# Performance work log

Measured on AMD Instinct MI355X. Metric: run time of the kernel, lower is better.

## Reference

```python
import jax, jax.numpy as jnp
import numpy as np

N_FILTERS = 40
FILTER_SIZE = 401   # int(16000*25/1000), forced odd
POOL_STRIDE = 160   # int(16000*10/1000)
EPS = 1e-6
S_SMOOTH = 0.04     # fixed PCEN smoothing coefficient s
DELTA = 2.0         # fixed PCEN bias delta
R_MIN, R_MAX = 0.2, 1.0
HIDDEN = 32


def setup_inputs() -> dict:
    key = jax.random.key(0)
    ks = jax.random.split(key, 6)
    B, L = 8, 160000
    x = jax.random.normal(ks[0], (B, L), dtype=jnp.float32)
    # mel-initialized Gabor params (as in mel_filter_params)
    sr, fmin, fmax = 16000.0, 60.0, 7800.0
    min_mel = 1127.0 * np.log1p(fmin / 700.0)
    max_mel = 1127.0 * np.log1p(fmax / 700.0)
    peaks_mel = np.linspace(min_mel, max_mel, N_FILTERS + 2)
    peaks_hz = 700.0 * np.expm1(peaks_mel / 1127.0)
    center_freqs = jnp.asarray(peaks_hz[1:-1] * 2.0 * np.pi / sr, dtype=jnp.float32)
    z = np.sqrt(2.0 * np.log(2.0)) / np.pi
    bandwidths = jnp.asarray(z * sr / (peaks_hz[2:] - peaks_hz[:-2]), dtype=jnp.float32)
    pooling_widths = jnp.full((N_FILTERS,), 0.4, dtype=jnp.float32)
    # GRU (input_size=1, hidden=32) + head Linear(32,32)->ReLU->Linear(32,2)
    def gl(k, shape):
        return jax.random.normal(k, shape, dtype=jnp.float32) * 0.1
    w_ih = gl(ks[1], (3 * HIDDEN, 1))
    w_hh = gl(ks[2], (3 * HIDDEN, HIDDEN))
    b_ih = jnp.zeros((3 * HIDDEN,), jnp.float32)
    b_hh = jnp.zeros((3 * HIDDEN,), jnp.float32)
    hw1 = gl(ks[3], (32, HIDDEN)); hb1 = jnp.zeros((32,), jnp.float32)
    hw2 = gl(ks[4], (2, 32)); hb2 = jnp.zeros((2,), jnp.float32)
    return dict(x=x, center_freqs=center_freqs, bandwidths=bandwidths,
                pooling_widths=pooling_widths, w_ih=w_ih, w_hh=w_hh,
                b_ih=b_ih, b_hh=b_hh, hw1=hw1, hb1=hb1, hw2=hw2, hb2=hb2)


def _gabor_filterbank(x, center_freqs, bandwidths, pooling_widths):
    z = np.sqrt(2.0 * np.log(2.0)) / np.pi
    cf = jnp.clip(center_freqs, 0.0, np.pi)
    bw = jnp.clip(bandwidths, 4.0 * z, FILTER_SIZE * z)
    t = jnp.arange(-(FILTER_SIZE // 2), (FILTER_SIZE + 1) // 2, dtype=jnp.float32)
    denom = 1.0 / (jnp.sqrt(2.0 * np.pi) * bw)                        # [F]
    gauss = jnp.exp(-(t[None, :] ** 2) / (2.0 * bw[:, None] ** 2))    # [F,K]
    phase = cf[:, None] * t[None, :]                                  # [F,K]
    fr = denom[:, None] * gauss * jnp.cos(phase)
    fi = denom[:, None] * gauss * jnp.sin(phase)
    filt = jnp.concatenate([fr, fi], axis=0)[:, None, :]              # [2F,1,K]
    pad = FILTER_SIZE // 2
    y = jax.lax.conv_general_dilated(x[:, None, :], filt, (1,), [(pad, pad)])
    y = y ** 2
    y = y[:, :N_FILTERS] + y[:, N_FILTERS:]                           # squared modulus [B,F,L]
    pw = jnp.clip(pooling_widths, 2.0 / FILTER_SIZE, 0.5)
    tt = jnp.arange(FILTER_SIZE, dtype=jnp.float32) / (FILTER_SIZE - 1) - 0.5
    win = jnp.exp(-0.5 * (tt[None, :] / pw[:, None]) ** 2)[:, None, :]  # [F,1,K]
    y = jax.lax.conv_general_dilated(y, win, (POOL_STRIDE,), [(pad, pad)],
                                     feature_group_count=N_FILTERS)
    return y  # [B,F,T]


def _gru_cell(h, xin, w_ih, w_hh, b_ih, b_hh):
    gi = xin @ w_ih.T + b_ih   # [N,3H]
    gh = h @ w_hh.T + b_hh
    i_r, i_z, i_n = jnp.split(gi, 3, axis=-1)
    h_r, h_z, h_n = jnp.split(gh, 3, axis=-1)
    r = jax.nn.sigmoid(i_r + h_r)
    zz = jax.nn.sigmoid(i_z + h_z)
    n = jnp.tanh(i_n + r * h_n)
    return (1.0 - zz) * n + zz * h


def _adaptive_pcen(frames, w_ih, w_hh, b_ih, b_hh, hw1, hb1, hw2, hb2):
    B, F, T = frames.shape
    Xt = jnp.transpose(frames, (2, 0, 1))  # [T,B,F]

    def controller(x_prev, x_t):  # each [B,F] -> per-bin (alpha, r)
        xp = x_prev.reshape(-1, 1)
        xc = x_t.reshape(-1, 1)
        h = jnp.zeros((B * F, HIDDEN), frames.dtype)
        h = _gru_cell(h, xp, w_ih, w_hh, b_ih, b_hh)
        h = _gru_cell(h, xc, w_ih, w_hh, b_ih, b_hh)
        hid = jax.nn.relu(h @ hw1.T + hb1)
        logits = hid @ hw2.T + hb2  # [B*F,2]
        alpha = jax.nn.sigmoid(logits[:, 0]).reshape(B, F)
        r = (R_MIN + (R_MAX - R_MIN) * jax.nn.sigmoid(logits[:, 1])).reshape(B, F)
        return alpha, r

    def step(carry, X_t):
        M_prev, X_prev = carry
        alpha, r = controller(X_prev, X_t)
        M_t = (1.0 - S_SMOOTH) * M_prev + S_SMOOTH * X_t
        out = (X_t / (M_t + EPS) ** alpha + DELTA) ** r - DELTA ** r
        return (M_t, X_t), out

    init = (jnp.zeros((B, F), frames.dtype), Xt[0])
    _, outs = jax.lax.scan(step, init, Xt)
    return jnp.transpose(outs, (1, 2, 0))  # [B,F,T]


def reference(x, center_freqs, bandwidths, pooling_widths,
              w_ih, w_hh, b_ih, b_hh, hw1, hb1, hw2, hb2):
    frames = _gabor_filterbank(x, center_freqs, bandwidths, pooling_widths)
    return _adaptive_pcen(frames, w_ih, w_hh, b_ih, b_hh, hw1, hb1, hw2, hb2)
```

## Files before the change

### kernel.cpp

```cpp
#include <hip/hip_runtime.h>
#include <math.h>

#define NF 40
#define FS 401
#define AST 424
#define PSTRIDE 160
#define BB 8
#define LL 160000
#define PADL 256
#define LST 160512
#define TOUT 1000
#define NTILE 256
#define NCHUNKC 625
#define ROWCH 89
#define ROWST (ROWCH*8)
#define TCP 16
#define NCHUNKP 63

typedef __attribute__((ext_vector_type(8))) _Float16 half8v;
typedef __attribute__((ext_vector_type(4))) _Float16 half4v;
typedef __attribute__((ext_vector_type(4))) float float4v;
typedef _Float16 f16;

__device__ __forceinline__ float sigm(float x) { return 1.0f / (1.0f + __expf(-x)); }
__device__ __forceinline__ float tanh_fast(float x) { return 1.0f - 2.0f / (__expf(2.0f * x) + 1.0f); }

__global__ __launch_bounds__(256) void prep_filters(
    const float* __restrict__ cf_, const float* __restrict__ bw_, f16* __restrict__ Ag)
{
    const float PI_F = 3.14159265358979323846f;
    int row = blockIdx.x;
    int f = row >> 1, comp = row & 1;
    float Z = sqrtf(2.0f * logf(2.0f)) / PI_F;
    float cf = fminf(fmaxf(cf_[f], 0.0f), PI_F);
    float bw = fminf(fmaxf(bw_[f], 4.0f * Z), 401.0f * Z);
    float denom = 1.0f / (sqrtf(2.0f * PI_F) * bw);
    float inv2 = 1.0f / (2.0f * bw * bw);
    for (int k = threadIdx.x; k < AST; k += 256) {
        float v = 0.0f;
        if (k < FS) {
            float t = (float)(k - 200);
            float g = denom * expf(-(t * t) * inv2);
            float sv, cv;
            sincosf(cf * t, &sv, &cv);
            v = comp ? g * sv : g * cv;
        }
        Ag[row * AST + k] = (f16)v;
    }
}

__global__ __launch_bounds__(256) void convert_x(
    const float* __restrict__ x, f16* __restrict__ xb)
{
    int i = blockIdx.x * 256 + threadIdx.x;
    if (i >= BB * LST) return;
    int b = i / LST, o = i % LST;
    float v = 0.0f;
    if (o >= PADL && o < PADL + LL) v = x[b * LL + (o - PADL)];
    xb[i] = (f16)v;
}

__global__ __launch_bounds__(256) void conv_mfma(
    const f16* __restrict__ xb,
    const f16* __restrict__ Ag,
    f16* __restrict__ eb)
{
    __shared__ f16 rows_[8 * ROWST];
    int chunk = blockIdx.x;
    int bi = blockIdx.y;
    int p0 = chunk * NTILE;
    int pbase = PADL + p0 - 200;
    const f16* xs = xb + (size_t)bi * LST;
    int tid = threadIdx.x;

    for (int sc = tid; sc < 8 * 84; sc += 256) {
        int r = sc / 84, m = sc - r * 84;
        int s0 = pbase + 8 * m + (r & ~1);
        const uint* gp = (const uint*)(xs + s0);
        uint v0 = gp[0], v1 = gp[1], v2 = gp[2], v3 = gp[3], v4 = gp[4];
        if (r & 1) {
            v0 = __builtin_amdgcn_alignbyte(v1, v0, 2);
            v1 = __builtin_amdgcn_alignbyte(v2, v1, 2);
            v2 = __builtin_amdgcn_alignbyte(v3, v2, 2);
            v3 = __builtin_amdgcn_alignbyte(v4, v3, 2);
        }
        *(uint4*)(&rows_[r * ROWST + 8 * m]) = make_uint4(v0, v1, v2, v3);
    }
    __syncthreads();

    int wv = tid >> 6, lane = tid & 63, q = lane >> 4, l15 = lane & 15;

    float4v acc[5][4];
#pragma unroll
    for (int t = 0; t < 5; ++t)
#pragma unroll
        for (int s = 0; s < 4; ++s)
            acc[t][s] = (float4v){0.f, 0.f, 0.f, 0.f};

    const f16* aP[5];
    const f16* bP[4];
#pragma unroll
    for (int t = 0; t < 5; ++t) aP[t] = Ag + (16 * t + l15) * AST + 8 * q;
#pragma unroll
    for (int s = 0; s < 4; ++s) {
        int pos = 64 * wv + 16 * s + l15;
        bP[s] = rows_ + (pos & 7) * ROWST + 8 * ((pos >> 3) + q);
    }

    for (int k = 0; k < 416; k += 32) {
        half8v af[5], bf[4];
#pragma unroll
        for (int t = 0; t < 5; ++t) af[t] = *(const half8v*)(aP[t] + k);
#pragma unroll
        for (int s = 0; s < 4; ++s) bf[s] = *(const half8v*)(bP[s] + k);
#pragma unroll
        for (int t = 0; t < 5; ++t)
#pragma unroll
            for (int s = 0; s < 4; ++s)
                acc[t][s] = __builtin_amdgcn_mfma_f32_16x16x32_f16(af[t], bf[s], acc[t][s], 0, 0, 0);
    }

    f16* ebb = eb + (size_t)bi * NF * LL;
#pragma unroll
    for (int t = 0; t < 5; ++t) {
        int f0 = 8 * t + 2 * q;
#pragma unroll
        for (int s = 0; s < 4; ++s) {
            float4v a = acc[t][s];
            int p = p0 + 64 * wv + 16 * s + l15;
            float e0 = a.x * a.x + a.y * a.y;
            float e1 = a.z * a.z + a.w * a.w;
            ebb[f0 * LL + p] = (f16)e0;
            ebb[(f0 + 1) * LL + p] = (f16)e1;
        }
    }
}

__global__ __launch_bounds__(256) void pool_kernel(
    const f16* __restrict__ eb, const float* __restrict__ pw_, float* __restrict__ Xout)
{
    __shared__ float ys[2816];
    __shared__ float win[416];
    int chunk = blockIdx.x;
    int f = blockIdx.y;
    int bi = blockIdx.z;
    int tau0 = chunk * TCP;
    int start = tau0 * PSTRIDE - 200;
    int tid = threadIdx.x;

    float pw = fminf(fmaxf(pw_[f], 2.0f / 401.0f), 0.5f);
    float invpw = 1.0f / pw;
    for (int k = tid; k < 416; k += 256) {
        float w = 0.0f;
        if (k < FS) {
            float tt = (float)k * (1.0f / 400.0f) - 0.5f;
            float u = tt * invpw;
            w = expf(-0.5f * u * u);
        }
        win[k] = w;
    }
    const f16* erow = eb + ((size_t)bi * NF + f) * LL;
    if (start >= 0 && start + 2816 <= LL) {
        for (int j = tid; j < 352; j += 256) {
            half8v v = *(const half8v*)(erow + start + 8 * j);
#pragma unroll
            for (int i = 0; i < 8; ++i) ys[8 * j + i] = (float)v[i];
        }
    } else {
        for (int j = tid; j < 2816; j += 256) {
            int p = start + j;
            ys[j] = (p >= 0 && p < LL) ? (float)erow[p] : 0.0f;
        }
    }
    __syncthreads();

    int ft = tid >> 4, l16 = tid & 15;
    float acc = 0.0f;
    int yo = ft * PSTRIDE;
    for (int kw = l16; kw < FS; kw += 16)
        acc += ys[yo + kw] * win[kw];
#pragma unroll
    for (int off = 8; off > 0; off >>= 1)
        acc += __shfl_down(acc, off, 16);
    int tau = tau0 + ft;
    if (l16 == 0 && tau < TOUT)
        Xout[((size_t)bi * NF + f) * TOUT + tau] = acc;
}

__global__ __launch_bounds__(256) void pcen_scan_kernel(
    const float* __restrict__ X, float* __restrict__ M)
{
    int wid = (blockIdx.x * 256 + threadIdx.x) >> 6;
    int lane = threadIdx.x & 63;
    if (wid >= BB * NF) return;
    const float a1 = 0.96f;
    const float a2 = a1 * a1;
    const float a4 = a2 * a2;
    const float a8 = a4 * a4;
    const float a16 = a8 * a8;
    const float a32 = a16 * a16;
    const float ss = 0.04f;
    float al1 = powf(a1, (float)(lane + 1));
    float carry = 0.0f;
    const float* row = X + wid * TOUT;
    float* mrow = M + wid * TOUT;

    for (int c = 0; c < TOUT; c += 64) {
        int t = c + lane;
        float v = (t < TOUT) ? row[t] : 0.0f;
        float y = ss * v;
        float u;
        u = __shfl_up(y, 1, 64);  if (lane >= 1)  y = fmaf(a1, u, y);
        u = __shfl_up(y, 2, 64);  if (lane >= 2)  y = fmaf(a2, u, y);
        u = __shfl_up(y, 4, 64);  if (lane >= 4)  y = fmaf(a4, u, y);
        u = __shfl_up(y, 8, 64);  if (lane >= 8)  y = fmaf(a8, u, y);
        u = __shfl_up(y, 16, 64); if (lane >= 16) y = fmaf(a16, u, y);
        u = __shfl_up(y, 32, 64); if (lane >= 32) y = fmaf(a32, u, y);
        y = fmaf(al1, carry, y);
        carry = __shfl(y, 63, 64);
        if (t < TOUT) mrow[t] = y;
    }
}

__global__ __launch_bounds__(256) void pcen_ctrl_mfma(
    const float* __restrict__ X, const float* __restrict__ M,
    const float* __restrict__ w_ih, const float* __restrict__ w_hh,
    const float* __restrict__ b_ih, const float* __restrict__ b_hh,
    const float* __restrict__ hw1, const float* __restrict__ hb1,
    const float* __restrict__ hw2, const float* __restrict__ hb2,
    float* __restrict__ out)
{
    __shared__ f16 s_whhA[96 * 40];
    __shared__ f16 s_w1A[32 * 40];
    __shared__ __align__(16) float4 s_A1[32];
    __shared__ __align__(16) float4 s_A2[32];
    __shared__ float s_hb1[32];
    __shared__ float s_hw2[64];
    __shared__ float s_hb2[2];
    __shared__ f16 sh1[4][16 * 40];
    __shared__ f16 sh2[4][16 * 40];
    __shared__ float sxc[4][16], sxp[4][16], smv[4][16];

    int tid = threadIdx.x;
    for (int i = tid; i < 96 * 32; i += 256) {
        int m = i >> 5, k = i & 31;
        s_whhA[m * 40 + k] = (f16)w_hh[i];
    }
    for (int i = tid; i < 32 * 32; i += 256) {
        int m = i >> 5, k = i & 31;
        s_w1A[m * 40 + k] = (f16)hw1[i];
    }
    if (tid < 32) {
        int j = tid;
        s_A1[j] = make_float4(w_ih[j], b_ih[j] + b_hh[j],
                              w_ih[32 + j], b_ih[32 + j] + b_hh[32 + j]);
        s_A2[j] = make_float4(w_ih[64 + j], b_ih[64 + j], b_hh[64 + j], 0.0f);
        s_hb1[j] = hb1[j];
    }
    if (tid < 64) s_hw2[tid] = hw2[tid];
    if (tid < 2)  s_hb2[tid] = hb2[tid];
    __syncthreads();

    int wv = tid >> 6, lane = tid & 63;
    int c = lane & 15, q = lane >> 4;
    int instBase = blockIdx.x * 64 + wv * 16;

    if (lane < 16) {
        int idx = instBase + lane;
        int t = idx % TOUT;
        float xcv = X[idx];
        float xpv = (t == 0) ? xcv : X[idx - 1];
        sxc[wv][lane] = xcv;
        sxp[wv][lane] = xpv;
        smv[wv][lane] = M[idx];
    }
    float xp = sxp[wv][c];
    float xc = sxc[wv][c];
    float mv = smv[wv][c];

    float h1v[8];
#pragma unroll
    for (int jj = 0; jj < 8; ++jj) {
        int j = (jj < 4) ? (4 * q + jj) : (16 + 4 * q + (jj - 4));
        float4 a1 = s_A1[j];
        float4 a2 = s_A2[j];
        float r = sigm(fmaf(xp, a1.x, a1.y));
        float z = sigm(fmaf(xp, a1.z, a1.w));
        float n = tanh_fast(fmaf(xp, a2.x, a2.y) + r * a2.z);
        h1v[jj] = (1.0f - z) * n;
    }

    {
        half4v lo = {(f16)h1v[0], (f16)h1v[1], (f16)h1v[2], (f16)h1v[3]};
        half4v hi = {(f16)h1v[4], (f16)h1v[5], (f16)h1v[6], (f16)h1v[7]};
        *(half4v*)(&sh1[wv][c * 40 + 4 * q]) = lo;
        *(half4v*)(&sh1[wv][c * 40 + 16 + 4 * q]) = hi;
    }

    float4v acc[6];
    {
        half8v bf = *(const half8v*)(&sh1[wv][c * 40 + 8 * q]);
#pragma unroll
        for (int t = 0; t < 6; ++t) {
            half8v af = *(const half8v*)(&s_whhA[(16 * t + c) * 40 + 8 * q]);
            acc[t] = __builtin_amdgcn_mfma_f32_16x16x32_f16(af, bf, (float4v){0.f,0.f,0.f,0.f}, 0, 0, 0);
        }
    }

    float h2v[8];
#pragma unroll
    for (int jj = 0; jj < 8; ++jj) {
        int j = (jj < 4) ? (4 * q + jj) : (16 + 4 * q + (jj - 4));
        int reg = jj & 3;
        float accR = (jj < 4) ? acc[0][reg] : acc[1][reg];
        float accZ = (jj < 4) ? acc[2][reg] : acc[3][reg];
        float accN = (jj < 4) ? acc[4][reg] : acc[5][reg];
        float4 a1 = s_A1[j];
        float4 a2 = s_A2[j];
        float r = sigm(fmaf(xc, a1.x, a1.y) + accR);
        float z = sigm(fmaf(xc, a1.z, a1.w) + accZ);
        float gn = accN + a2.z;
        float n = tanh_fast(fmaf(xc, a2.x, a2.y) + r * gn);
        h2v[jj] = fmaf(z, h1v[jj] - n, n);
    }

    {
        half4v lo = {(f16)h2v[0], (f16)h2v[1], (f16)h2v[2], (f16)h2v[3]};
        half4v hi = {(f16)h2v[4], (f16)h2v[5], (f16)h2v[6], (f16)h2v[7]};
        *(half4v*)(&sh2[wv][c * 40 + 4 * q]) = lo;
        *(half4v*)(&sh2[wv][c * 40 + 16 + 4 * q]) = hi;
    }

    float4v hacc[2];
    {
        half8v bf = *(const half8v*)(&sh2[wv][c * 40 + 8 * q]);
#pragma unroll
        for (int t = 0; t < 2; ++t) {
            half8v af = *(const half8v*)(&s_w1A[(16 * t + c) * 40 + 8 * q]);
            hacc[t] = __builtin_amdgcn_mfma_f32_16x16x32_f16(af, bf, (float4v){0.f,0.f,0.f,0.f}, 0, 0, 0);
        }
    }

    float p0 = 0.f, p1 = 0.f;
#pragma unroll
    for (int jj = 0; jj < 8; ++jj) {
        int i = (jj < 4) ? (4 * q + jj) : (16 + 4 * q + (jj - 4));
        int reg = jj & 3;
        float hv = (jj < 4) ? hacc[0][reg] : hacc[1][reg];
        hv = fmaxf(hv + s_hb1[i], 0.0f);
        p0 = fmaf(hv, s_hw2[i], p0);
        p1 = fmaf(hv, s_hw2[32 + i], p1);
    }
    p0 += __shfl_xor(p0, 16);
    p0 += __shfl_xor(p0, 32);
    p1 += __shfl_xor(p1, 16);
    p1 += __shfl_xor(p1, 32);

    float alpha = sigm(p0 + s_hb2[0]);
    float rr = fmaf(0.8f, sigm(p1 + s_hb2[1]), 0.2f);
    float md = __expf(alpha * __logf(mv + 1e-6f));
    float bse = xc / md + 2.0f;
    float val = __expf(rr * __logf(bse)) - __expf(rr * 0.69314718056f);
    if (lane < 16)
        out[instBase + lane] = val;
}

extern "C" void kernel_launch(void* const* d_in, const int* in_sizes, int n_in,
                              void* d_out, int out_size, void* d_ws, size_t ws_size,
                              hipStream_t stream) {
    const float* x    = (const float*)d_in[0];
    const float* cf   = (const float*)d_in[1];
    const float* bw   = (const float*)d_in[2];
    const float* pw   = (const float*)d_in[3];
    const float* w_ih = (const float*)d_in[4];
    const float* w_hh = (const float*)d_in[5];
    const float* b_ih = (const float*)d_in[6];
    const float* b_hh = (const float*)d_in[7];
    const float* hw1  = (const float*)d_in[8];
    const float* hb1  = (const float*)d_in[9];
    const float* hw2  = (const float*)d_in[10];
    const float* hb2  = (const float*)d_in[11];
    float* out = (float*)d_out;

    const size_t xb_b  = (size_t)BB * LST * 2;
    const size_t ag_b  = (size_t)80 * AST * 2;
    const size_t xm_b  = (size_t)2 * BB * NF * TOUT * 4;
    size_t fixed = xb_b + ag_b + xm_b;
    size_t e_per_batch = (size_t)NF * LL * 2;
    int nb;
    if (ws_size >= fixed + 8 * e_per_batch)      nb = 8;
    else if (ws_size >= fixed + 2 * e_per_batch) nb = 2;
    else                                         nb = 1;
    int nslice = BB / nb;

    f16* xb   = (f16*)d_ws;
    f16* Ag   = xb + (size_t)BB * LST;
    f16* ebuf = Ag + (size_t)80 * AST;
    float* Xf = (float*)(ebuf + (size_t)nb * NF * LL);
    float* Mf = Xf + (size_t)BB * NF * TOUT;

    prep_filters<<<dim3(80), dim3(256), 0, stream>>>(cf, bw, Ag);
    convert_x<<<dim3((BB * LST + 255) / 256), dim3(256), 0, stream>>>(x, xb);

    for (int sl = 0; sl < nslice; ++sl) {
        conv_mfma<<<dim3(NCHUNKC, nb), dim3(256), 0, stream>>>(
            xb + (size_t)sl * nb * LST, Ag, ebuf);
        pool_kernel<<<dim3(NCHUNKP, NF, nb), dim3(256), 0, stream>>>(
            ebuf, pw, Xf + (size_t)sl * nb * NF * TOUT);
    }

    pcen_scan_kernel<<<dim3((BB * NF * 64) / 256), dim3(256), 0, stream>>>(Xf, Mf);
    pcen_ctrl_mfma<<<dim3((BB * NF * TOUT) / 64), dim3(256), 0, stream>>>(
        Xf, Mf, w_ih, w_hh, b_ih, b_hh, hw1, hb1, hw2, hb2, out);
}
```

Measured before the change: 293.3 us.

## Fuse Gabor conv energy with Gaussian pooling via LDS and atomic accumulation

Merges the conv_mfma and pool_kernel passes into one kernel. Each block computes squared-magnitude energies for a 512-sample tile into LDS and pools them directly with atomicAdd partial sums into the frame output. This removes the large f16 energy buffer written to and read back from global memory, and the per-slice launch loop. The tile per block doubles, which raises register pressure (40 accumulators per lane), and it adds a memset, a window-precompute kernel and float atomics whose summation order is nondeterministic. The pooling loop is scalar and serial per thread, and only 240 of 256 threads do it.

New measurement: 312.2 us. 1.06x slower.

```diff
diff --git a/kernel.cpp b/kernel.cpp
--- a/kernel.cpp
+++ b/kernel.cpp
@@ -8,14 +8,16 @@
 #define BB 8
 #define LL 160000
 #define PADL 256
-#define LST 160512
+#define PADR 512
+#define LST 160768
 #define TOUT 1000
-#define NTILE 256
-#define NCHUNKC 625
-#define ROWCH 89
+#define NTILE 512
+#define NCHUNKC 313
+#define ROWCH 121
 #define ROWST (ROWCH*8)
-#define TCP 16
-#define NCHUNKP 63
+#define EST 518
+#define WST 402
+#define WOFF 41472
 
 typedef __attribute__((ext_vector_type(8))) _Float16 half8v;
 typedef __attribute__((ext_vector_type(4))) _Float16 half4v;
@@ -49,6 +51,23 @@
     }
 }
 
+__global__ __launch_bounds__(256) void prep_win(
+    const float* __restrict__ pw_, f16* __restrict__ winG)
+{
+    int f = blockIdx.x;
+    float pw = fminf(fmaxf(pw_[f], 2.0f / 401.0f), 0.5f);
+    float invpw = 1.0f / pw;
+    for (int j = threadIdx.x; j < WST; j += 256) {
+        float w = 0.0f;
+        if (j < FS) {
+            float tt = (float)j * (1.0f / 400.0f) - 0.5f;
+            float u = tt * invpw;
+            w = expf(-0.5f * u * u);
+        }
+        winG[f * WST + j] = (f16)w;
+    }
+}
+
 __global__ __launch_bounds__(256) void convert_x(
     const float* __restrict__ x, f16* __restrict__ xb)
 {
@@ -60,12 +79,17 @@
     xb[i] = (f16)v;
 }
 
-__global__ __launch_bounds__(256) void conv_mfma(
+__global__ __launch_bounds__(256, 2) void conv_pool(
     const f16* __restrict__ xb,
     const f16* __restrict__ Ag,
-    f16* __restrict__ eb)
-{
-    __shared__ f16 rows_[8 * ROWST];
+    const f16* __restrict__ winG,
+    float* __restrict__ Xout)
+{
+    __shared__ __align__(16) unsigned char smem[WOFF + 20 * WST * 2];
+    f16* slab = (f16*)smem;
+    f16* eL   = (f16*)smem;
+    f16* wL   = (f16*)(smem + WOFF);
+
     int chunk = blockIdx.x;
     int bi = blockIdx.y;
     int p0 = chunk * NTILE;
@@ -73,8 +97,8 @@
     const f16* xs = xb + (size_t)bi * LST;
     int tid = threadIdx.x;
 
-    for (int sc = tid; sc < 8 * 84; sc += 256) {
-        int r = sc / 84, m = sc - r * 84;
+    for (int sc = tid; sc < 8 * 117; sc += 256) {
+        int r = sc / 117, m = sc - r * 117;
         int s0 = pbase + 8 * m + (r & ~1);
         const uint* gp = (const uint*)(xs + s0);
         uint v0 = gp[0], v1 = gp[1], v2 = gp[2], v3 = gp[3], v4 = gp[4];
@@ -84,107 +108,89 @@
             v2 = __builtin_amdgcn_alignbyte(v3, v2, 2);
             v3 = __builtin_amdgcn_alignbyte(v4, v3, 2);
         }
-        *(uint4*)(&rows_[r * ROWST + 8 * m]) = make_uint4(v0, v1, v2, v3);
+        *(uint4*)(&slab[r * ROWST + 8 * m]) = make_uint4(v0, v1, v2, v3);
     }
     __syncthreads();
 
     int wv = tid >> 6, lane = tid & 63, q = lane >> 4, l15 = lane & 15;
 
-    float4v acc[5][4];
+    float4v acc[5][8];
 #pragma unroll
     for (int t = 0; t < 5; ++t)
 #pragma unroll
-        for (int s = 0; s < 4; ++s)
+        for (int s = 0; s < 8; ++s)
             acc[t][s] = (float4v){0.f, 0.f, 0.f, 0.f};
 
     const f16* aP[5];
-    const f16* bP[4];
+    const f16* bP[8];
 #pragma unroll
     for (int t = 0; t < 5; ++t) aP[t] = Ag + (16 * t + l15) * AST + 8 * q;
 #pragma unroll
-    for (int s = 0; s < 4; ++s) {
-        int pos = 64 * wv + 16 * s + l15;
-        bP[s] = rows_ + (pos & 7) * ROWST + 8 * ((pos >> 3) + q);
+    for (int s = 0; s < 8; ++s) {
+        int pos = 128 * wv + 16 * s + l15;
+        bP[s] = slab + (pos & 7) * ROWST + 8 * ((pos >> 3) + q);
     }
 
     for (int k = 0; k < 416; k += 32) {
-        half8v af[5], bf[4];
+        half8v af[5], bf[8];
 #pragma unroll
         for (int t = 0; t < 5; ++t) af[t] = *(const half8v*)(aP[t] + k);
 #pragma unroll
-        for (int s = 0; s < 4; ++s) bf[s] = *(const half8v*)(bP[s] + k);
+        for (int s = 0; s < 8; ++s) bf[s] = *(const half8v*)(bP[s] + k);
 #pragma unroll
         for (int t = 0; t < 5; ++t)
 #pragma unroll
-            for (int s = 0; s < 4; ++s)
+            for (int s = 0; s < 8; ++s)
                 acc[t][s] = __builtin_amdgcn_mfma_f32_16x16x32_f16(af[t], bf[s], acc[t][s], 0, 0, 0);
     }
 
-    f16* ebb = eb + (size_t)bi * NF * LL;
+    __syncthreads();
+
 #pragma unroll
     for (int t = 0; t < 5; ++t) {
         int f0 = 8 * t + 2 * q;
 #pragma unroll
-        for (int s = 0; s < 4; ++s) {
+        for (int s = 0; s < 8; ++s) {
             float4v a = acc[t][s];
-            int p = p0 + 64 * wv + 16 * s + l15;
-            float e0 = a.x * a.x + a.y * a.y;
-            float e1 = a.z * a.z + a.w * a.w;
-            ebb[f0 * LL + p] = (f16)e0;
-            ebb[(f0 + 1) * LL + p] = (f16)e1;
-        }
-    }
-}
-
-__global__ __launch_bounds__(256) void pool_kernel(
-    const f16* __restrict__ eb, const float* __restrict__ pw_, float* __restrict__ Xout)
-{
-    __shared__ float ys[2816];
-    __shared__ float win[416];
-    int chunk = blockIdx.x;
-    int f = blockIdx.y;
-    int bi = blockIdx.z;
-    int tau0 = chunk * TCP;
-    int start = tau0 * PSTRIDE - 200;
-    int tid = threadIdx.x;
-
-    float pw = fminf(fmaxf(pw_[f], 2.0f / 401.0f), 0.5f);
-    float invpw = 1.0f / pw;
-    for (int k = tid; k < 416; k += 256) {
-        float w = 0.0f;
-        if (k < FS) {
-            float tt = (float)k * (1.0f / 400.0f) - 0.5f;
-            float u = tt * invpw;
-            w = expf(-0.5f * u * u);
-        }
-        win[k] = w;
-    }
-    const f16* erow = eb + ((size_t)bi * NF + f) * LL;
-    if (start >= 0 && start + 2816 <= LL) {
-        for (int j = tid; j < 352; j += 256) {
-            half8v v = *(const half8v*)(erow + start + 8 * j);
-#pragma unroll
-            for (int i = 0; i < 8; ++i) ys[8 * j + i] = (float)v[i];
-        }
-    } else {
-        for (int j = tid; j < 2816; j += 256) {
-            int p = start + j;
-            ys[j] = (p >= 0 && p < LL) ? (float)erow[p] : 0.0f;
+            int pl = 128 * wv + 16 * s + l15;
+            eL[f0 * EST + pl] = (f16)(a.x * a.x + a.y * a.y);
+            eL[(f0 + 1) * EST + pl] = (f16)(a.z * a.z + a.w * a.w);
         }
     }
     __syncthreads();
 
-    int ft = tid >> 4, l16 = tid & 15;
-    float acc = 0.0f;
-    int yo = ft * PSTRIDE;
-    for (int kw = l16; kw < FS; kw += 16)
-        acc += ys[yo + kw] * win[kw];
-#pragma unroll
-    for (int off = 8; off > 0; off >>= 1)
-        acc += __shfl_down(acc, off, 16);
-    int tau = tau0 + ft;
-    if (l16 == 0 && tau < TOUT)
-        Xout[((size_t)bi * NF + f) * TOUT + tau] = acc;
+    int tau_lo = (p0 > 200) ? (p0 - 200 + 159) / 160 : 0;
+    float* Xb = Xout + (size_t)bi * NF * TOUT;
+
+    for (int ph = 0; ph < 2; ++ph) {
+        const uint4* src = (const uint4*)(winG + ph * 20 * WST);
+        uint4* dst = (uint4*)wL;
+        for (int u = tid; u < (20 * WST * 2) / 16; u += 256) dst[u] = src[u];
+        __syncthreads();
+
+        if (tid < 240) {
+            int fl = tid / 12, r = tid % 12, ti = r >> 1, h = r & 1;
+            int f = ph * 20 + fl;
+            int tau = tau_lo + ti;
+            if (tau < TOUT) {
+                int base = tau * PSTRIDE - 200;
+                int jlo = max(0, p0 - base);
+                int jhi = min(401, p0 + NTILE - base);
+                int jm = (jlo + jhi + 1) >> 1;
+                int ja = h ? jm : jlo;
+                int jb = h ? jhi : jm;
+                if (ja < jb) {
+                    float a = 0.0f;
+                    const f16* er = eL + f * EST + (base - p0);
+                    const f16* wr = wL + fl * WST;
+                    for (int j = ja; j < jb; ++j)
+                        a = fmaf((float)er[j], (float)wr[j], a);
+                    atomicAdd(&Xb[f * TOUT + tau], a);
+                }
+            }
+        }
+        __syncthreads();
+    }
 }
 
 __global__ __launch_bounds__(256) void pcen_scan_kernel(
@@ -382,32 +388,18 @@
     const float* hb2  = (const float*)d_in[11];
     float* out = (float*)d_out;
 
-    const size_t xb_b  = (size_t)BB * LST * 2;
-    const size_t ag_b  = (size_t)80 * AST * 2;
-    const size_t xm_b  = (size_t)2 * BB * NF * TOUT * 4;
-    size_t fixed = xb_b + ag_b + xm_b;
-    size_t e_per_batch = (size_t)NF * LL * 2;
-    int nb;
-    if (ws_size >= fixed + 8 * e_per_batch)      nb = 8;
-    else if (ws_size >= fixed + 2 * e_per_batch) nb = 2;
-    else                                         nb = 1;
-    int nslice = BB / nb;
-
-    f16* xb   = (f16*)d_ws;
-    f16* Ag   = xb + (size_t)BB * LST;
-    f16* ebuf = Ag + (size_t)80 * AST;
-    float* Xf = (float*)(ebuf + (size_t)nb * NF * LL);
-    float* Mf = Xf + (size_t)BB * NF * TOUT;
+    f16* xb    = (f16*)d_ws;
+    f16* Ag    = xb + (size_t)BB * LST;
+    f16* winG  = Ag + (size_t)80 * AST;
+    float* Xf  = (float*)(winG + (size_t)NF * WST);
+    float* Mf  = Xf + (size_t)BB * NF * TOUT;
 
     prep_filters<<<dim3(80), dim3(256), 0, stream>>>(cf, bw, Ag);
+    prep_win<<<dim3(NF), dim3(256), 0, stream>>>(pw, winG);
     convert_x<<<dim3((BB * LST + 255) / 256), dim3(256), 0, stream>>>(x, xb);
-
-    for (int sl = 0; sl < nslice; ++sl) {
-        conv_mfma<<<dim3(NCHUNKC, nb), dim3(256), 0, stream>>>(
-            xb + (size_t)sl * nb * LST, Ag, ebuf);
-        pool_kernel<<<dim3(NCHUNKP, NF, nb), dim3(256), 0, stream>>>(
-            ebuf, pw, Xf + (size_t)sl * nb * NF * TOUT);
-    }
+    hipMemsetAsync(Xf, 0, (size_t)BB * NF * TOUT * sizeof(float), stream);
+
+    conv_pool<<<dim3(NCHUNKC, BB), dim3(256), 0, stream>>>(xb, Ag, winG, Xf);
 
     pcen_scan_kernel<<<dim3((BB * NF * 64) / 256), dim3(256), 0, stream>>>(Xf, Mf);
     pcen_ctrl_mfma<<<dim3((BB * NF * TOUT) / 64), dim3(256), 0, stream>>>(
```

## Double conv MFMA output tile per block and merge prep kernels into one launch

Applied to the files above, without the earlier changes.

The convolution tile grows from 256 to 512 output positions per block. Each wave now computes 8 position subtiles, so every filter A-fragment loaded is reused across twice as many MFMAs, and the shared-memory slab grows to match. The input padding is widened and a bounds check guards the partial last tile. The x-to-f16 conversion and filter preparation are merged into a single launch to remove one kernel launch. The trade-off is more accumulator registers (occupancy is pinned at 2 blocks per CU via launch bounds) and fewer blocks in the grid.

Measured after the change: 310.8 us. 1.06x slower.

```diff
diff --git a/kernel.cpp b/kernel.cpp
--- a/kernel.cpp
+++ b/kernel.cpp
@@ -8,14 +8,16 @@
 #define BB 8
 #define LL 160000
 #define PADL 256
-#define LST 160512
+#define PADR 512
+#define LST 160768
 #define TOUT 1000
-#define NTILE 256
-#define NCHUNKC 625
-#define ROWCH 89
+#define NTILE 512
+#define NCHUNKC 313
+#define ROWCH 121
 #define ROWST (ROWCH*8)
 #define TCP 16
 #define NCHUNKP 63
+#define NCONVB 5024
 
 typedef __attribute__((ext_vector_type(8))) _Float16 half8v;
 typedef __attribute__((ext_vector_type(4))) _Float16 half4v;
@@ -25,11 +27,21 @@
 __device__ __forceinline__ float sigm(float x) { return 1.0f / (1.0f + __expf(-x)); }
 __device__ __forceinline__ float tanh_fast(float x) { return 1.0f - 2.0f / (__expf(2.0f * x) + 1.0f); }
 
-__global__ __launch_bounds__(256) void prep_filters(
-    const float* __restrict__ cf_, const float* __restrict__ bw_, f16* __restrict__ Ag)
+__global__ __launch_bounds__(256) void prep_all(
+    const float* __restrict__ x, const float* __restrict__ cf_,
+    const float* __restrict__ bw_, f16* __restrict__ xb, f16* __restrict__ Ag)
 {
+    int blk = blockIdx.x;
+    if (blk < NCONVB) {
+        int i = blk * 256 + threadIdx.x;
+        int b = i / LST, o = i % LST;
+        float v = 0.0f;
+        if (o >= PADL && o < PADL + LL) v = x[b * LL + (o - PADL)];
+        xb[i] = (f16)v;
+        return;
+    }
     const float PI_F = 3.14159265358979323846f;
-    int row = blockIdx.x;
+    int row = blk - NCONVB;
     int f = row >> 1, comp = row & 1;
     float Z = sqrtf(2.0f * logf(2.0f)) / PI_F;
     float cf = fminf(fmaxf(cf_[f], 0.0f), PI_F);
@@ -49,23 +61,12 @@
     }
 }
 
-__global__ __launch_bounds__(256) void convert_x(
-    const float* __restrict__ x, f16* __restrict__ xb)
-{
-    int i = blockIdx.x * 256 + threadIdx.x;
-    if (i >= BB * LST) return;
-    int b = i / LST, o = i % LST;
-    float v = 0.0f;
-    if (o >= PADL && o < PADL + LL) v = x[b * LL + (o - PADL)];
-    xb[i] = (f16)v;
-}
-
-__global__ __launch_bounds__(256) void conv_mfma(
+__global__ __launch_bounds__(256, 2) void conv_mfma(
     const f16* __restrict__ xb,
     const f16* __restrict__ Ag,
     f16* __restrict__ eb)
 {
-    __shared__ f16 rows_[8 * ROWST];
+    __shared__ f16 slab[8 * ROWST];
     int chunk = blockIdx.x;
     int bi = blockIdx.y;
     int p0 = chunk * NTILE;
@@ -73,8 +74,8 @@
     const f16* xs = xb + (size_t)bi * LST;
     int tid = threadIdx.x;
 
-    for (int sc = tid; sc < 8 * 84; sc += 256) {
-        int r = sc / 84, m = sc - r * 84;
+    for (int sc = tid; sc < 8 * 117; sc += 256) {
+        int r = sc / 117, m = sc - r * 117;
         int s0 = pbase + 8 * m + (r & ~1);
         const uint* gp = (const uint*)(xs + s0);
         uint v0 = gp[0], v1 = gp[1], v2 = gp[2], v3 = gp[3], v4 = gp[4];
@@ -84,39 +85,39 @@
             v2 = __builtin_amdgcn_alignbyte(v3, v2, 2);
             v3 = __builtin_amdgcn_alignbyte(v4, v3, 2);
         }
-        *(uint4*)(&rows_[r * ROWST + 8 * m]) = make_uint4(v0, v1, v2, v3);
+        *(uint4*)(&slab[r * ROWST + 8 * m]) = make_uint4(v0, v1, v2, v3);
     }
     __syncthreads();
 
     int wv = tid >> 6, lane = tid & 63, q = lane >> 4, l15 = lane & 15;
 
-    float4v acc[5][4];
+    float4v acc[5][8];
 #pragma unroll
     for (int t = 0; t < 5; ++t)
 #pragma unroll
-        for (int s = 0; s < 4; ++s)
+        for (int s = 0; s < 8; ++s)
             acc[t][s] = (float4v){0.f, 0.f, 0.f, 0.f};
 
     const f16* aP[5];
-    const f16* bP[4];
+    const f16* bP[8];
 #pragma unroll
     for (int t = 0; t < 5; ++t) aP[t] = Ag + (16 * t + l15) * AST + 8 * q;
 #pragma unroll
-    for (int s = 0; s < 4; ++s) {
-        int pos = 64 * wv + 16 * s + l15;
-        bP[s] = rows_ + (pos & 7) * ROWST + 8 * ((pos >> 3) + q);
+    for (int s = 0; s < 8; ++s) {
+        int pos = 128 * wv + 16 * s + l15;
+        bP[s] = slab + (pos & 7) * ROWST + 8 * ((pos >> 3) + q);
     }
 
     for (int k = 0; k < 416; k += 32) {
-        half8v af[5], bf[4];
+        half8v af[5], bf[8];
 #pragma unroll
         for (int t = 0; t < 5; ++t) af[t] = *(const half8v*)(aP[t] + k);
 #pragma unroll
-        for (int s = 0; s < 4; ++s) bf[s] = *(const half8v*)(bP[s] + k);
+        for (int s = 0; s < 8; ++s) bf[s] = *(const half8v*)(bP[s] + k);
 #pragma unroll
         for (int t = 0; t < 5; ++t)
 #pragma unroll
-            for (int s = 0; s < 4; ++s)
+            for (int s = 0; s < 8; ++s)
                 acc[t][s] = __builtin_amdgcn_mfma_f32_16x16x32_f16(af[t], bf[s], acc[t][s], 0, 0, 0);
     }
 
@@ -125,13 +126,13 @@
     for (int t = 0; t < 5; ++t) {
         int f0 = 8 * t + 2 * q;
 #pragma unroll
-        for (int s = 0; s < 4; ++s) {
+        for (int s = 0; s < 8; ++s) {
             float4v a = acc[t][s];
-            int p = p0 + 64 * wv + 16 * s + l15;
-            float e0 = a.x * a.x + a.y * a.y;
-            float e1 = a.z * a.z + a.w * a.w;
-            ebb[f0 * LL + p] = (f16)e0;
-            ebb[(f0 + 1) * LL + p] = (f16)e1;
+            int p = p0 + 128 * wv + 16 * s + l15;
+            if (p < LL) {
+                ebb[f0 * LL + p] = (f16)(a.x * a.x + a.y * a.y);
+                ebb[(f0 + 1) * LL + p] = (f16)(a.z * a.z + a.w * a.w);
+            }
         }
     }
 }
@@ -382,9 +383,9 @@
     const float* hb2  = (const float*)d_in[11];
     float* out = (float*)d_out;
 
-    const size_t xb_b  = (size_t)BB * LST * 2;
-    const size_t ag_b  = (size_t)80 * AST * 2;
-    const size_t xm_b  = (size_t)2 * BB * NF * TOUT * 4;
+    const size_t xb_b = (size_t)BB * LST * 2;
+    const size_t ag_b = (size_t)80 * AST * 2;
+    const size_t xm_b = (size_t)2 * BB * NF * TOUT * 4;
     size_t fixed = xb_b + ag_b + xm_b;
     size_t e_per_batch = (size_t)NF * LL * 2;
     int nb;
@@ -399,8 +400,7 @@
     float* Xf = (float*)(ebuf + (size_t)nb * NF * LL);
     float* Mf = Xf + (size_t)BB * NF * TOUT;
 
-    prep_filters<<<dim3(80), dim3(256), 0, stream>>>(cf, bw, Ag);
-    convert_x<<<dim3((BB * LST + 255) / 256), dim3(256), 0, stream>>>(x, xb);
+    prep_all<<<dim3(NCONVB + 80), dim3(256), 0, stream>>>(x, cf, bw, xb, Ag);
 
     for (int sl = 0; sl < nslice; ++sl) {
         conv_mfma<<<dim3(NCHUNKC, nb), dim3(256), 0, stream>>>(
```
